# Kernel tuning notes

Measured on AMD Instinct MI355X. Metric: run time of the kernel, lower is better.

## Reference

```python
import jax, jax.numpy as jnp
import numpy as np

NEG_SLOPE = 0.2
EPS = 1e-16

def gatv2(x, edge_index, edge_attr, Wl, bl, We, att, bias):
    """PyG GATv2Conv, heads=1, share_weights=True, with edge_dim."""
    N = x.shape[0]
    h = x @ Wl + bl                      # [N, out] shared lin_l == lin_r
    src, dst = edge_index[0], edge_index[1]
    hj = h[src]                          # source (message) features [E, out]
    hi = h[dst]                          # target features [E, out]
    e = jax.nn.leaky_relu(hi + hj + edge_attr @ We, NEG_SLOPE)  # [E, out]
    score = e @ att                      # [E]
    # segment softmax over edges grouped by destination node
    smax = jax.ops.segment_max(score, dst, num_segments=N)
    ex = jnp.exp(score - smax[dst])
    denom = jax.ops.segment_sum(ex, dst, num_segments=N)
    alpha = ex / (denom[dst] + EPS)      # [E]
    out = jax.ops.segment_sum(hj * alpha[:, None], dst, num_segments=N)
    return out + bias


def setup_inputs() -> dict:
    key = jax.random.key(0)
    N, E = 50000, 800000
    D_IN, D_LAT, D_EDGE, N_ACT = 128, 128, 16, 32
    ks = jax.random.split(key, 16)
    s = 0.05
    inp = {
        "x": jax.random.normal(ks[0], (N, D_IN), jnp.float32),
        "edge_index": jax.random.randint(ks[1], (2, E), 0, N, jnp.int32),
        "edge_attr": jax.random.normal(ks[2], (E, D_EDGE), jnp.float32),
        # gnn_layer: D_IN -> D_LAT
        "Wl1": jax.random.normal(ks[3], (D_IN, D_LAT), jnp.float32) * s,
        "bl1": jnp.zeros((D_LAT,), jnp.float32),
        "We1": jax.random.normal(ks[4], (D_EDGE, D_LAT), jnp.float32) * s,
        "att1": jax.random.normal(ks[5], (D_LAT,), jnp.float32) * s,
        "bias1": jnp.zeros((D_LAT,), jnp.float32),
        # node_layer: D_LAT -> 1
        "Wl2": jax.random.normal(ks[6], (D_LAT, 1), jnp.float32) * s,
        "bl2": jnp.zeros((1,), jnp.float32),
        "We2": jax.random.normal(ks[7], (D_EDGE, 1), jnp.float32) * s,
        "att2": jax.random.normal(ks[8], (1,), jnp.float32) * s,
        "bias2": jnp.zeros((1,), jnp.float32),
        # action_layer: D_LAT -> N_ACT
        "Wl3": jax.random.normal(ks[9], (D_LAT, N_ACT), jnp.float32) * s,
        "bl3": jnp.zeros((N_ACT,), jnp.float32),
        "We3": jax.random.normal(ks[10], (D_EDGE, N_ACT), jnp.float32) * s,
        "att3": jax.random.normal(ks[11], (N_ACT,), jnp.float32) * s,
        "bias3": jnp.zeros((N_ACT,), jnp.float32),
    }
    return inp


def reference(x, edge_index, edge_attr,
              Wl1, bl1, We1, att1, bias1,
              Wl2, bl2, We2, att2, bias2,
              Wl3, bl3, We3, att3, bias3):
    latent = gatv2(x, edge_index, edge_attr, Wl1, bl1, We1, att1, bias1)          # [N, D_LAT]
    node_logits = gatv2(latent, edge_index, edge_attr, Wl2, bl2, We2, att2, bias2)[:, 0]  # [N]
    action_logits = gatv2(latent, edge_index, edge_attr, Wl3, bl3, We3, att3, bias3)      # [N, A]
    # categorical sampling with fixed key (deterministic reference)
    k1, k2 = jax.random.split(jax.random.key(42))
    node_sel = jax.random.categorical(k1, node_logits)
    node_lp = jax.nn.log_softmax(node_logits)[node_sel]
    act_logits_sel = action_logits[node_sel, :]
    action_sel = jax.random.categorical(k2, act_logits_sel)
    action_lp = jax.nn.log_softmax(act_logits_sel)[action_sel]
    return (node_sel, action_sel, node_lp + action_lp)
```

## Files before the change

### kernel.cpp

```cpp
#include <hip/hip_runtime.h>
#include <stdint.h>
#include <math.h>

#define NEG 0.2f
#define TINYF 1.1754943508222875e-38f

__host__ __device__ inline void threefry2x32(uint32_t k0, uint32_t k1,
                                             uint32_t x0, uint32_t x1,
                                             uint32_t* o0, uint32_t* o1) {
  uint32_t ks0 = k0, ks1 = k1, ks2 = k0 ^ k1 ^ 0x1BD11BDAu;
  x0 += ks0; x1 += ks1;
#define RR(r) { x0 += x1; x1 = (x1 << (r)) | (x1 >> (32 - (r))); x1 ^= x0; }
  RR(13) RR(15) RR(26) RR(6)
  x0 += ks1; x1 += ks2 + 1u;
  RR(17) RR(29) RR(16) RR(24)
  x0 += ks2; x1 += ks0 + 2u;
  RR(13) RR(15) RR(26) RR(6)
  x0 += ks0; x1 += ks1 + 3u;
  RR(17) RR(29) RR(16) RR(24)
  x0 += ks1; x1 += ks2 + 4u;
  RR(13) RR(15) RR(26) RR(6)
  x0 += ks2; x1 += ks0 + 5u;
#undef RR
  *o0 = x0; *o1 = x1;
}

__device__ inline float gumbel_part(uint32_t ka, uint32_t kb, uint32_t i) {
  uint32_t o0, o1;
  threefry2x32(ka, kb, 0u, i, &o0, &o1);
  uint32_t bits = o0 ^ o1;
  float f = __uint_as_float((bits >> 9) | 0x3f800000u) - 1.0f;
  float u = fmaxf(TINYF, f + TINYF);
  return -logf(-logf(u));
}

__global__ void count_kernel(const int* __restrict__ ei, int E, int* __restrict__ counts) {
  int e = blockIdx.x * blockDim.x + threadIdx.x;
  if (e < E) atomicAdd(&counts[ei[E + e]], 1);
}

__global__ __launch_bounds__(1024) void scan_kernel(const int* __restrict__ counts,
    int* __restrict__ row_start, int* __restrict__ cursor, int N, int E) {
  __shared__ int wsum[16];
  __shared__ int base_s;
  int tid = threadIdx.x;
  int lane = tid & 63, wv = tid >> 6;
  if (tid == 0) base_s = 0;
  __syncthreads();
  for (int chunk = 0; chunk < N; chunk += 1024) {
    int i = chunk + tid;
    int v = (i < N) ? counts[i] : 0;
    int incl = v;
#pragma unroll
    for (int off = 1; off < 64; off <<= 1) {
      int t = __shfl_up(incl, off);
      if (lane >= off) incl += t;
    }
    if (lane == 63) wsum[wv] = incl;
    __syncthreads();
    if (wv == 0) {
      int x = (lane < 16) ? wsum[lane] : 0;
#pragma unroll
      for (int off = 1; off < 16; off <<= 1) {
        int t = __shfl_up(x, off);
        if (lane >= off) x += t;
      }
      if (lane < 16) wsum[lane] = x;
    }
    __syncthreads();
    int waveoff = (wv == 0) ? 0 : wsum[wv - 1];
    int base = base_s;
    int excl = base + waveoff + incl - v;
    if (i < N) { row_start[i] = excl; cursor[i] = excl; }
    __syncthreads();
    if (tid == 1023) base_s = base + wsum[15];
    __syncthreads();
  }
  if (tid == 0) row_start[N] = base_s;
}

__global__ void scatter_kernel(const int* __restrict__ ei, const float* __restrict__ ea,
                               int E, int* __restrict__ cursor,
                               int* __restrict__ src_csr, float* __restrict__ ea_csr) {
  int e = blockIdx.x * blockDim.x + threadIdx.x;
  if (e < E) {
    int d = ei[E + e];
    int p = atomicAdd(&cursor[d], 1);
    src_csr[p] = ei[e];
    const float4* s4 = (const float4*)&ea[(size_t)e * 16];
    float4* d4 = (float4*)&ea_csr[(size_t)p * 16];
    float4 t0 = s4[0], t1 = s4[1], t2 = s4[2], t3 = s4[3];
    d4[0] = t0; d4[1] = t1; d4[2] = t2; d4[3] = t3;
  }
}

__global__ __launch_bounds__(256) void gemm128_kernel(const float* __restrict__ X,
    const float* __restrict__ W, const float* __restrict__ bias,
    float* __restrict__ out, int M) {
  __shared__ float xs[128][33];
  int row0 = blockIdx.x * 32;
  int tid = threadIdx.x;
  for (int idx = tid; idx < 32 * 128; idx += 256) {
    int r = idx >> 7;
    int k = idx & 127;
    int row = row0 + r;
    xs[k][r] = (row < M) ? X[(size_t)row * 128 + k] : 0.0f;
  }
  __syncthreads();
  int tc = tid & 31, tr = tid >> 5;
  int c0 = tc * 4, r0 = tr * 4;
  float acc[4][4] = {};
#pragma unroll 4
  for (int k = 0; k < 128; k++) {
    float4 w = *(const float4*)&W[k * 128 + c0];
    float x0 = xs[k][r0], x1 = xs[k][r0 + 1], x2 = xs[k][r0 + 2], x3 = xs[k][r0 + 3];
    acc[0][0] += x0 * w.x; acc[0][1] += x0 * w.y; acc[0][2] += x0 * w.z; acc[0][3] += x0 * w.w;
    acc[1][0] += x1 * w.x; acc[1][1] += x1 * w.y; acc[1][2] += x1 * w.z; acc[1][3] += x1 * w.w;
    acc[2][0] += x2 * w.x; acc[2][1] += x2 * w.y; acc[2][2] += x2 * w.z; acc[2][3] += x2 * w.w;
    acc[3][0] += x3 * w.x; acc[3][1] += x3 * w.y; acc[3][2] += x3 * w.z; acc[3][3] += x3 * w.w;
  }
  float4 b4 = *(const float4*)&bias[c0];
  for (int r = 0; r < 4; r++) {
    int row = row0 + r0 + r;
    if (row < M) {
      float4 o;
      o.x = acc[r][0] + b4.x; o.y = acc[r][1] + b4.y;
      o.z = acc[r][2] + b4.z; o.w = acc[r][3] + b4.w;
      *(float4*)&out[(size_t)row * 128 + c0] = o;
    }
  }
}

__global__ __launch_bounds__(256) void gemm32_kernel(const float* __restrict__ X,
    const float* __restrict__ W, const float* __restrict__ bias,
    float* __restrict__ out, int M) {
  int t = blockIdx.x * 256 + threadIdx.x;
  int node = t >> 5, c = t & 31;
  if (node >= M) return;
  const float4* xp = (const float4*)&X[(size_t)node * 128];
  float acc = 0.f;
#pragma unroll
  for (int q = 0; q < 32; q++) {
    float4 x4 = xp[q];
    acc += x4.x * W[(q * 4 + 0) * 32 + c] + x4.y * W[(q * 4 + 1) * 32 + c]
         + x4.z * W[(q * 4 + 2) * 32 + c] + x4.w * W[(q * 4 + 3) * 32 + c];
  }
  out[(size_t)node * 32 + c] = acc + bias[c];
}

__global__ __launch_bounds__(256) void gemv_kernel(const float* __restrict__ X,
    const float* __restrict__ w, const float* __restrict__ b0,
    float* __restrict__ out, int M) {
  int wv = (blockIdx.x * 256 + threadIdx.x) >> 6;
  int lane = threadIdx.x & 63;
  if (wv >= M) return;
  float2 xv = *(const float2*)&X[(size_t)wv * 128 + lane * 2];
  float2 wvv = *(const float2*)&w[lane * 2];
  float v = xv.x * wvv.x + xv.y * wvv.y;
#pragma unroll
  for (int off = 32; off; off >>= 1) v += __shfl_xor(v, off);
  if (lane == 0) out[wv] = v + b0[0];
}

__global__ __launch_bounds__(256) void fused1_kernel(const float* __restrict__ h,
    const int* __restrict__ src_csr, const int* __restrict__ row_start,
    const float* __restrict__ ea_csr,
    const float* __restrict__ We, const float* __restrict__ att,
    const float* __restrict__ bias, float* __restrict__ out, int N) {
  __shared__ float WeS[2048];
  int tid = threadIdx.x;
  for (int i = tid; i < 2048; i += 256) WeS[i] = We[i];
  __syncthreads();
  int hw = (blockIdx.x * 256 + tid) >> 5;
  int lane = tid & 31;
  if (hw >= N) return;
  int c4 = lane * 4;
  float4 attv = *(const float4*)&att[c4];
  float4 b4 = *(const float4*)&bias[c4];
  int start = row_start[hw];
  int deg = row_start[hw + 1] - start;
  if (deg == 0) {
    *(float4*)&out[(size_t)hw * 128 + c4] = b4;
    return;
  }
  float4 hi = *(const float4*)&h[(size_t)hw * 128 + c4];
  int s_l = (lane < deg) ? src_csr[start + lane] : 0;
  int dcap = deg < 32 ? deg : 32;
  const float4* eap = (const float4*)&ea_csr[(size_t)start * 16];
  float m = -INFINITY, l = 0.f;
  float4 acc = make_float4(0.f, 0.f, 0.f, 0.f);
  for (int j = 0; j < deg; j++) {
    int s = (j < dcap) ? __shfl(s_l, j, 32) : src_csr[start + j];
    float4 hj = *(const float4*)&h[(size_t)s * 128 + c4];
    float4 v;
    v.x = hi.x + hj.x; v.y = hi.y + hj.y; v.z = hi.z + hj.z; v.w = hi.w + hj.w;
#pragma unroll
    for (int q = 0; q < 4; q++) {
      float4 aq = eap[(size_t)j * 4 + q];
      float4 w0 = *(const float4*)&WeS[(4 * q + 0) * 128 + c4];
      float4 w1 = *(const float4*)&WeS[(4 * q + 1) * 128 + c4];
      float4 w2 = *(const float4*)&WeS[(4 * q + 2) * 128 + c4];
      float4 w3 = *(const float4*)&WeS[(4 * q + 3) * 128 + c4];
      v.x += aq.x * w0.x + aq.y * w1.x + aq.z * w2.x + aq.w * w3.x;
      v.y += aq.x * w0.y + aq.y * w1.y + aq.z * w2.y + aq.w * w3.y;
      v.z += aq.x * w0.z + aq.y * w1.z + aq.z * w2.z + aq.w * w3.z;
      v.w += aq.x * w0.w + aq.y * w1.w + aq.z * w2.w + aq.w * w3.w;
    }
    v.x = v.x >= 0.f ? v.x : NEG * v.x;
    v.y = v.y >= 0.f ? v.y : NEG * v.y;
    v.z = v.z >= 0.f ? v.z : NEG * v.z;
    v.w = v.w >= 0.f ? v.w : NEG * v.w;
    float sc = v.x * attv.x + v.y * attv.y + v.z * attv.z + v.w * attv.w;
#pragma unroll
    for (int off = 16; off; off >>= 1) sc += __shfl_xor(sc, off);
    float mn = fmaxf(m, sc);
    float scale = __expf(m - mn);
    float w = __expf(sc - mn);
    l = l * scale + w;
    acc.x = acc.x * scale + w * hj.x;
    acc.y = acc.y * scale + w * hj.y;
    acc.z = acc.z * scale + w * hj.z;
    acc.w = acc.w * scale + w * hj.w;
    m = mn;
  }
  float inv = 1.0f / (l + 1e-16f);
  float4 o;
  o.x = acc.x * inv + b4.x;
  o.y = acc.y * inv + b4.y;
  o.z = acc.z * inv + b4.z;
  o.w = acc.w * inv + b4.w;
  *(float4*)&out[(size_t)hw * 128 + c4] = o;
}

__global__ __launch_bounds__(256) void fused23_kernel(
    const float* __restrict__ h3, const float* __restrict__ h2,
    const int* __restrict__ src_csr, const int* __restrict__ row_start,
    const float* __restrict__ ea_csr,
    const float* __restrict__ We3, const float* __restrict__ att3,
    const float* __restrict__ bias3, const float* __restrict__ We2,
    const float* __restrict__ att2, const float* __restrict__ bias2,
    float* __restrict__ out3, float* __restrict__ logits, int N) {
  __shared__ float We3S[512];
  __shared__ float att3S[32];
  __shared__ float We2S[16];
  int tid = threadIdx.x;
  for (int i = tid; i < 512; i += 256) We3S[i] = We3[i];
  if (tid < 32) att3S[tid] = att3[tid];
  if (tid < 16) We2S[tid] = We2[tid];
  __syncthreads();
  int wv = (blockIdx.x * 256 + tid) >> 6;
  int lane = tid & 63;
  if (wv >= N) return;
  int c = lane & 31;
  int par = lane >> 5;
  float bi3 = bias3[c];
  int start = row_start[wv];
  int deg = row_start[wv + 1] - start;
  if (deg == 0) {
    if (par == 0) out3[(size_t)wv * 32 + c] = bi3;
    if (lane == 0) logits[wv] = bias2[0];
    return;
  }
  float at3 = att3S[c];
  float a2s = att2[0];
  float hi3 = h3[(size_t)wv * 32 + c];
  float hi2 = h2[wv];
  int s_l = (lane < deg) ? src_csr[start + lane] : 0;
  int dcap = deg < 64 ? deg : 64;
  const float4* eap = (const float4*)&ea_csr[(size_t)start * 16];
  float m3 = -INFINITY, l3 = 0.f, acc3 = 0.f;
  float m2 = -INFINITY, l2 = 0.f, acc2 = 0.f;
  for (int j = par; j < deg; j += 2) {
    int s = (j < dcap) ? __shfl(s_l, j) : src_csr[start + j];
    float hj3 = h3[(size_t)s * 32 + c];
    float h2s = h2[s];
    float4 c0 = eap[(size_t)j * 4 + 0];
    float4 c1 = eap[(size_t)j * 4 + 1];
    float4 c2 = eap[(size_t)j * 4 + 2];
    float4 c3 = eap[(size_t)j * 4 + 3];
    float v3 = hi3 + hj3;
    v3 += c0.x * We3S[0 * 32 + c]  + c0.y * We3S[1 * 32 + c]  + c0.z * We3S[2 * 32 + c]  + c0.w * We3S[3 * 32 + c];
    v3 += c1.x * We3S[4 * 32 + c]  + c1.y * We3S[5 * 32 + c]  + c1.z * We3S[6 * 32 + c]  + c1.w * We3S[7 * 32 + c];
    v3 += c2.x * We3S[8 * 32 + c]  + c2.y * We3S[9 * 32 + c]  + c2.z * We3S[10 * 32 + c] + c2.w * We3S[11 * 32 + c];
    v3 += c3.x * We3S[12 * 32 + c] + c3.y * We3S[13 * 32 + c] + c3.z * We3S[14 * 32 + c] + c3.w * We3S[15 * 32 + c];
    v3 = v3 >= 0.f ? v3 : NEG * v3;
    float t3 = v3 * at3;
#pragma unroll
    for (int off = 16; off; off >>= 1) t3 += __shfl_xor(t3, off);
    float v2 = hi2 + h2s;
    v2 += c0.x * We2S[0]  + c0.y * We2S[1]  + c0.z * We2S[2]  + c0.w * We2S[3];
    v2 += c1.x * We2S[4]  + c1.y * We2S[5]  + c1.z * We2S[6]  + c1.w * We2S[7];
    v2 += c2.x * We2S[8]  + c2.y * We2S[9]  + c2.z * We2S[10] + c2.w * We2S[11];
    v2 += c3.x * We2S[12] + c3.y * We2S[13] + c3.z * We2S[14] + c3.w * We2S[15];
    v2 = v2 >= 0.f ? v2 : NEG * v2;
    float t2 = v2 * a2s;
    float mn3 = fmaxf(m3, t3);
    float sc3 = __expf(m3 - mn3);
    float w3 = __expf(t3 - mn3);
    l3 = l3 * sc3 + w3;
    acc3 = acc3 * sc3 + w3 * hj3;
    m3 = mn3;
    float mn2 = fmaxf(m2, t2);
    float sc2 = __expf(m2 - mn2);
    float w2 = __expf(t2 - mn2);
    l2 = l2 * sc2 + w2;
    acc2 = acc2 * sc2 + w2 * h2s;
    m2 = mn2;
  }
  float m3o = __shfl_xor(m3, 32), l3o = __shfl_xor(l3, 32), acc3o = __shfl_xor(acc3, 32);
  float M3 = fmaxf(m3, m3o);
  float sA3 = (m3 == -INFINITY) ? 0.f : __expf(m3 - M3);
  float sB3 = (m3o == -INFINITY) ? 0.f : __expf(m3o - M3);
  float L3 = l3 * sA3 + l3o * sB3;
  float A3 = acc3 * sA3 + acc3o * sB3;
  float m2o = __shfl_xor(m2, 32), l2o = __shfl_xor(l2, 32), acc2o = __shfl_xor(acc2, 32);
  float M2 = fmaxf(m2, m2o);
  float sA2 = (m2 == -INFINITY) ? 0.f : __expf(m2 - M2);
  float sB2 = (m2o == -INFINITY) ? 0.f : __expf(m2o - M2);
  float L2 = l2 * sA2 + l2o * sB2;
  float A2 = acc2 * sA2 + acc2o * sB2;
  if (par == 0) out3[(size_t)wv * 32 + c] = A3 / (L3 + 1e-16f) + bi3;
  if (lane == 0) logits[wv] = A2 / (L2 + 1e-16f) + bias2[0];
}

#define NSB 64
__global__ __launch_bounds__(256) void node_partial_kernel(const float* __restrict__ logits,
    int N, uint32_t ka, uint32_t kb,
    float* __restrict__ pB, int* __restrict__ pI,
    float* __restrict__ pM, float* __restrict__ pL) {
  int chunk = (N + NSB - 1) / NSB;
  int s0 = blockIdx.x * chunk;
  int s1 = s0 + chunk; if (s1 > N) s1 = N;
  int tid = threadIdx.x;
  float best = -INFINITY; int bi = 0x7fffffff;
  float m = -INFINITY, l = 0.f;
  for (int i = s0 + tid; i < s1; i += 256) {
    float lg = logits[i];
    float mn = fmaxf(m, lg);
    l = l * __expf(m - mn) + __expf(lg - mn);
    m = mn;
    float v = lg + gumbel_part(ka, kb, (uint32_t)i);
    if (v > best) { best = v; bi = i; }
  }
  __shared__ float sb[256], sm[256], sl[256];
  __shared__ int si[256];
  sb[tid] = best; si[tid] = bi; sm[tid] = m; sl[tid] = l;
  __syncthreads();
  for (int s = 128; s; s >>= 1) {
    if (tid < s) {
      if (sb[tid + s] > sb[tid] || (sb[tid + s] == sb[tid] && si[tid + s] < si[tid])) {
        sb[tid] = sb[tid + s]; si[tid] = si[tid + s];
      }
      float M = fmaxf(sm[tid], sm[tid + s]);
      float t0 = (sm[tid] == -INFINITY) ? 0.f : sl[tid] * __expf(sm[tid] - M);
      float t1 = (sm[tid + s] == -INFINITY) ? 0.f : sl[tid + s] * __expf(sm[tid + s] - M);
      sm[tid] = M; sl[tid] = t0 + t1;
    }
    __syncthreads();
  }
  if (tid == 0) { pB[blockIdx.x] = sb[0]; pI[blockIdx.x] = si[0]; pM[blockIdx.x] = sm[0]; pL[blockIdx.x] = sl[0]; }
}

__global__ __launch_bounds__(64) void node_final_kernel(const float* __restrict__ logits,
    const float* __restrict__ pB, const int* __restrict__ pI,
    const float* __restrict__ pM, const float* __restrict__ pL,
    float* __restrict__ scal) {
  int lane = threadIdx.x;
  float best = pB[lane]; int bi = pI[lane];
  float m = pM[lane]; float l = pL[lane];
#pragma unroll
  for (int off = 32; off; off >>= 1) {
    float ob = __shfl_xor(best, off); int oi = __shfl_xor(bi, off);
    if (ob > best || (ob == best && oi < bi)) { best = ob; bi = oi; }
    float om = __shfl_xor(m, off); float ol = __shfl_xor(l, off);
    float M = fmaxf(m, om);
    float t0 = (m == -INFINITY) ? 0.f : l * __expf(m - M);
    float t1 = (om == -INFINITY) ? 0.f : ol * __expf(om - M);
    m = M; l = t0 + t1;
  }
  if (lane == 0) {
    ((int*)scal)[0] = bi;
    scal[3] = logits[bi] - (m + logf(l));
  }
}

__global__ __launch_bounds__(64) void action_kernel(const float* __restrict__ out3,
    const float* __restrict__ scal, uint32_t ka, uint32_t kb,
    float* __restrict__ dout, int out_size) {
  int lane = threadIdx.x;
  int sel = ((const int*)scal)[0];
  float v = -INFINITY, noisy = -INFINITY;
  if (lane < 32) {
    v = out3[(size_t)sel * 32 + lane];
    noisy = v + gumbel_part(ka, kb, (uint32_t)lane);
  }
  int idx = lane;
  float nv = noisy;
#pragma unroll
  for (int off = 32; off; off >>= 1) {
    float ov = __shfl_xor(nv, off);
    int oi = __shfl_xor(idx, off);
    if (ov > nv || (ov == nv && oi < idx)) { nv = ov; idx = oi; }
  }
  float vm = v;
#pragma unroll
  for (int off = 32; off; off >>= 1) vm = fmaxf(vm, __shfl_xor(vm, off));
  float ex = (lane < 32) ? expf(v - vm) : 0.f;
#pragma unroll
  for (int off = 32; off; off >>= 1) ex += __shfl_xor(ex, off);
  float vsel = __shfl(v, idx);
  if (lane == 0) {
    float action_lp = vsel - vm - logf(ex);
    dout[0] = (float)sel;
    dout[1] = (float)idx;
    dout[2] = scal[3] + action_lp;
  }
  for (int i = 3 + lane; i < out_size; i += 64) dout[i] = 0.f;
}

extern "C" void kernel_launch(void* const* d_in, const int* in_sizes, int n_in,
                              void* d_out, int out_size, void* d_ws, size_t ws_size,
                              hipStream_t stream) {
  const float* x     = (const float*)d_in[0];
  const int*   ei    = (const int*)d_in[1];
  const float* ea    = (const float*)d_in[2];
  const float* Wl1   = (const float*)d_in[3];
  const float* bl1   = (const float*)d_in[4];
  const float* We1   = (const float*)d_in[5];
  const float* att1  = (const float*)d_in[6];
  const float* bias1 = (const float*)d_in[7];
  const float* Wl2   = (const float*)d_in[8];
  const float* bl2   = (const float*)d_in[9];
  const float* We2   = (const float*)d_in[10];
  const float* att2  = (const float*)d_in[11];
  const float* bias2 = (const float*)d_in[12];
  const float* Wl3   = (const float*)d_in[13];
  const float* bl3   = (const float*)d_in[14];
  const float* We3   = (const float*)d_in[15];
  const float* att3  = (const float*)d_in[16];
  const float* bias3 = (const float*)d_in[17];
  int N = in_sizes[0] / 128;
  int E = in_sizes[1] / 2;
  float* out = (float*)d_out;

  char* p = (char*)d_ws;
  auto alloc = [&](size_t bytes) -> char* {
    char* r = p; p += (bytes + 255) & ~(size_t)255; return r;
  };
  float* h1      = (float*)alloc((size_t)N * 128 * 4);
  float* latent  = (float*)alloc((size_t)N * 128 * 4);
  float* h3      = (float*)alloc((size_t)N * 32 * 4);
  float* h2      = (float*)alloc((size_t)N * 4);
  float* logits  = (float*)alloc((size_t)N * 4);
  float* out3    = (float*)alloc((size_t)N * 32 * 4);
  int* counts    = (int*)alloc((size_t)N * 4);
  int* row_start = (int*)alloc((size_t)(N + 1) * 4);
  int* cursor    = (int*)alloc((size_t)N * 4);
  int* src_csr   = (int*)alloc((size_t)E * 4);
  float* ea_csr  = (float*)alloc((size_t)E * 16 * 4);
  float* pB      = (float*)alloc(NSB * 4);
  int*   pI      = (int*)alloc(NSB * 4);
  float* pM      = (float*)alloc(NSB * 4);
  float* pL      = (float*)alloc(NSB * 4);
  float* scal    = (float*)alloc(64);
  (void)ws_size; (void)n_in;

  uint32_t k1a, k1b, k2a, k2b;
  threefry2x32(0u, 42u, 0u, 0u, &k1a, &k1b);
  threefry2x32(0u, 42u, 0u, 1u, &k2a, &k2b);

  hipMemsetAsync(counts, 0, (size_t)N * 4, stream);
  count_kernel<<<(E + 255) / 256, 256, 0, stream>>>(ei, E, counts);
  scan_kernel<<<1, 1024, 0, stream>>>(counts, row_start, cursor, N, E);
  scatter_kernel<<<(E + 255) / 256, 256, 0, stream>>>(ei, ea, E, cursor, src_csr, ea_csr);

  gemm128_kernel<<<(N + 31) / 32, 256, 0, stream>>>(x, Wl1, bl1, h1, N);
  fused1_kernel<<<(N + 7) / 8, 256, 0, stream>>>(h1, src_csr, row_start,
                                                 ea_csr, We1, att1, bias1, latent, N);

  gemm32_kernel<<<((size_t)N * 32 + 255) / 256, 256, 0, stream>>>(latent, Wl3, bl3, h3, N);
  gemv_kernel<<<(N + 3) / 4, 256, 0, stream>>>(latent, Wl2, bl2, h2, N);

  fused23_kernel<<<(N + 3) / 4, 256, 0, stream>>>(h3, h2, src_csr, row_start, ea_csr,
                                                  We3, att3, bias3, We2, att2, bias2,
                                                  out3, logits, N);

  node_partial_kernel<<<NSB, 256, 0, stream>>>(logits, N, k1a, k1b, pB, pI, pM, pL);
  node_final_kernel<<<1, 64, 0, stream>>>(logits, pB, pI, pM, pL, scal);
  action_kernel<<<1, 64, 0, stream>>>(out3, scal, k2a, k2b, out, out_size);
}
```

Before: 665.8 us.

## Narrow per-node lane groups in fused edge-softmax kernels and register-cache edge weights

Layer-1 fused kernel now assigns 16 lanes per destination node with 8 channels each instead of 32 lanes with 4, so a wavefront covers four nodes and each lane issues more independent loads and FMAs. The layer-2/3 kernel splits edges across four 16-lane groups with two action channels per lane, holds We3/We2 in registers instead of LDS, and merges the online-softmax partial states through a two-step shuffle tree. The aim is more memory-level parallelism on the irregular gathers and fewer idle lanes on low-degree nodes, at the cost of higher register pressure and possibly lower occupancy.

```diff
diff --git a/kernel.cpp b/kernel.cpp
--- a/kernel.cpp
+++ b/kernel.cpp
@@ -171,65 +171,84 @@
   int tid = threadIdx.x;
   for (int i = tid; i < 2048; i += 256) WeS[i] = We[i];
   __syncthreads();
-  int hw = (blockIdx.x * 256 + tid) >> 5;
-  int lane = tid & 31;
-  if (hw >= N) return;
-  int c4 = lane * 4;
-  float4 attv = *(const float4*)&att[c4];
-  float4 b4 = *(const float4*)&bias[c4];
-  int start = row_start[hw];
-  int deg = row_start[hw + 1] - start;
+  int node = (blockIdx.x * 256 + tid) >> 4;
+  int l16 = tid & 15;
+  if (node >= N) return;
+  int c8 = l16 * 8;
+  float4 at0 = *(const float4*)&att[c8];
+  float4 at1 = *(const float4*)&att[c8 + 4];
+  float4 bb0 = *(const float4*)&bias[c8];
+  float4 bb1 = *(const float4*)&bias[c8 + 4];
+  int start = row_start[node];
+  int deg = row_start[node + 1] - start;
+  float* op = &out[(size_t)node * 128 + c8];
   if (deg == 0) {
-    *(float4*)&out[(size_t)hw * 128 + c4] = b4;
+    *(float4*)op = bb0;
+    *(float4*)(op + 4) = bb1;
     return;
   }
-  float4 hi = *(const float4*)&h[(size_t)hw * 128 + c4];
-  int s_l = (lane < deg) ? src_csr[start + lane] : 0;
-  int dcap = deg < 32 ? deg : 32;
+  const float4* hp0 = (const float4*)&h[(size_t)node * 128 + c8];
+  float4 hi0 = hp0[0], hi1 = hp0[1];
+  int s_l = (l16 < deg) ? src_csr[start + l16] : 0;
+  int dcap = deg < 16 ? deg : 16;
   const float4* eap = (const float4*)&ea_csr[(size_t)start * 16];
   float m = -INFINITY, l = 0.f;
-  float4 acc = make_float4(0.f, 0.f, 0.f, 0.f);
+  float4 acc0 = make_float4(0.f, 0.f, 0.f, 0.f);
+  float4 acc1 = make_float4(0.f, 0.f, 0.f, 0.f);
   for (int j = 0; j < deg; j++) {
-    int s = (j < dcap) ? __shfl(s_l, j, 32) : src_csr[start + j];
-    float4 hj = *(const float4*)&h[(size_t)s * 128 + c4];
-    float4 v;
-    v.x = hi.x + hj.x; v.y = hi.y + hj.y; v.z = hi.z + hj.z; v.w = hi.w + hj.w;
+    int s = (j < dcap) ? __shfl(s_l, j, 16) : src_csr[start + j];
+    const float4* hjp = (const float4*)&h[(size_t)s * 128 + c8];
+    float4 hj0 = hjp[0], hj1 = hjp[1];
+    float4 v0, v1;
+    v0.x = hi0.x + hj0.x; v0.y = hi0.y + hj0.y; v0.z = hi0.z + hj0.z; v0.w = hi0.w + hj0.w;
+    v1.x = hi1.x + hj1.x; v1.y = hi1.y + hj1.y; v1.z = hi1.z + hj1.z; v1.w = hi1.w + hj1.w;
 #pragma unroll
     for (int q = 0; q < 4; q++) {
       float4 aq = eap[(size_t)j * 4 + q];
-      float4 w0 = *(const float4*)&WeS[(4 * q + 0) * 128 + c4];
-      float4 w1 = *(const float4*)&WeS[(4 * q + 1) * 128 + c4];
-      float4 w2 = *(const float4*)&WeS[(4 * q + 2) * 128 + c4];
-      float4 w3 = *(const float4*)&WeS[(4 * q + 3) * 128 + c4];
-      v.x += aq.x * w0.x + aq.y * w1.x + aq.z * w2.x + aq.w * w3.x;
-      v.y += aq.x * w0.y + aq.y * w1.y + aq.z * w2.y + aq.w * w3.y;
-      v.z += aq.x * w0.z + aq.y * w1.z + aq.z * w2.z + aq.w * w3.z;
-      v.w += aq.x * w0.w + aq.y * w1.w + aq.z * w2.w + aq.w * w3.w;
+#pragma unroll
+      for (int r = 0; r < 4; r++) {
+        int k = 4 * q + r;
+        float a = (r == 0) ? aq.x : (r == 1) ? aq.y : (r == 2) ? aq.z : aq.w;
+        float4 wa = *(const float4*)&WeS[k * 128 + c8];
+        float4 wb = *(const float4*)&WeS[k * 128 + c8 + 4];
+        v0.x += a * wa.x; v0.y += a * wa.y; v0.z += a * wa.z; v0.w += a * wa.w;
+        v1.x += a * wb.x; v1.y += a * wb.y; v1.z += a * wb.z; v1.w += a * wb.w;
+      }
     }
-    v.x = v.x >= 0.f ? v.x : NEG * v.x;
-    v.y = v.y >= 0.f ? v.y : NEG * v.y;
-    v.z = v.z >= 0.f ? v.z : NEG * v.z;
-    v.w = v.w >= 0.f ? v.w : NEG * v.w;
-    float sc = v.x * attv.x + v.y * attv.y + v.z * attv.z + v.w * attv.w;
-#pragma unroll
-    for (int off = 16; off; off >>= 1) sc += __shfl_xor(sc, off);
+    v0.x = v0.x >= 0.f ? v0.x : NEG * v0.x;
+    v0.y = v0.y >= 0.f ? v0.y : NEG * v0.y;
+    v0.z = v0.z >= 0.f ? v0.z : NEG * v0.z;
+    v0.w = v0.w >= 0.f ? v0.w : NEG * v0.w;
+    v1.x = v1.x >= 0.f ? v1.x : NEG * v1.x;
+    v1.y = v1.y >= 0.f ? v1.y : NEG * v1.y;
+    v1.z = v1.z >= 0.f ? v1.z : NEG * v1.z;
+    v1.w = v1.w >= 0.f ? v1.w : NEG * v1.w;
+    float sc = v0.x * at0.x + v0.y * at0.y + v0.z * at0.z + v0.w * at0.w
+             + v1.x * at1.x + v1.y * at1.y + v1.z * at1.z + v1.w * at1.w;
+#pragma unroll
+    for (int off = 8; off; off >>= 1) sc += __shfl_xor(sc, off);
     float mn = fmaxf(m, sc);
     float scale = __expf(m - mn);
     float w = __expf(sc - mn);
     l = l * scale + w;
-    acc.x = acc.x * scale + w * hj.x;
-    acc.y = acc.y * scale + w * hj.y;
-    acc.z = acc.z * scale + w * hj.z;
-    acc.w = acc.w * scale + w * hj.w;
+    acc0.x = acc0.x * scale + w * hj0.x;
+    acc0.y = acc0.y * scale + w * hj0.y;
+    acc0.z = acc0.z * scale + w * hj0.z;
+    acc0.w = acc0.w * scale + w * hj0.w;
+    acc1.x = acc1.x * scale + w * hj1.x;
+    acc1.y = acc1.y * scale + w * hj1.y;
+    acc1.z = acc1.z * scale + w * hj1.z;
+    acc1.w = acc1.w * scale + w * hj1.w;
     m = mn;
   }
   float inv = 1.0f / (l + 1e-16f);
-  float4 o;
-  o.x = acc.x * inv + b4.x;
-  o.y = acc.y * inv + b4.y;
-  o.z = acc.z * inv + b4.z;
-  o.w = acc.w * inv + b4.w;
-  *(float4*)&out[(size_t)hw * 128 + c4] = o;
+  float4 o0, o1;
+  o0.x = acc0.x * inv + bb0.x; o0.y = acc0.y * inv + bb0.y;
+  o0.z = acc0.z * inv + bb0.z; o0.w = acc0.w * inv + bb0.w;
+  o1.x = acc1.x * inv + bb1.x; o1.y = acc1.y * inv + bb1.y;
+  o1.z = acc1.z * inv + bb1.z; o1.w = acc1.w * inv + bb1.w;
+  *(float4*)op = o0;
+  *(float4*)(op + 4) = o1;
 }
 
 __global__ __launch_bounds__(256) void fused23_kernel(
@@ -240,87 +259,106 @@
     const float* __restrict__ bias3, const float* __restrict__ We2,
     const float* __restrict__ att2, const float* __restrict__ bias2,
     float* __restrict__ out3, float* __restrict__ logits, int N) {
-  __shared__ float We3S[512];
-  __shared__ float att3S[32];
-  __shared__ float We2S[16];
   int tid = threadIdx.x;
-  for (int i = tid; i < 512; i += 256) We3S[i] = We3[i];
-  if (tid < 32) att3S[tid] = att3[tid];
-  if (tid < 16) We2S[tid] = We2[tid];
-  __syncthreads();
   int wv = (blockIdx.x * 256 + tid) >> 6;
   int lane = tid & 63;
   if (wv >= N) return;
-  int c = lane & 31;
-  int par = lane >> 5;
-  float bi3 = bias3[c];
+  int q4 = lane >> 4;
+  int l16 = lane & 15;
+  int c2 = l16 * 2;
+  float2 we3[16];
+#pragma unroll
+  for (int k = 0; k < 16; k++) we3[k] = *(const float2*)&We3[k * 32 + c2];
+  float we2[16];
+#pragma unroll
+  for (int k = 0; k < 16; k++) we2[k] = We2[k];
+  float2 at3 = *(const float2*)&att3[c2];
+  float a2s = att2[0];
+  float2 bi3 = *(const float2*)&bias3[c2];
   int start = row_start[wv];
   int deg = row_start[wv + 1] - start;
   if (deg == 0) {
-    if (par == 0) out3[(size_t)wv * 32 + c] = bi3;
+    if (lane < 16) *(float2*)&out3[(size_t)wv * 32 + c2] = bi3;
     if (lane == 0) logits[wv] = bias2[0];
     return;
   }
-  float at3 = att3S[c];
-  float a2s = att2[0];
-  float hi3 = h3[(size_t)wv * 32 + c];
+  float2 hi3 = *(const float2*)&h3[(size_t)wv * 32 + c2];
   float hi2 = h2[wv];
   int s_l = (lane < deg) ? src_csr[start + lane] : 0;
   int dcap = deg < 64 ? deg : 64;
   const float4* eap = (const float4*)&ea_csr[(size_t)start * 16];
-  float m3 = -INFINITY, l3 = 0.f, acc3 = 0.f;
-  float m2 = -INFINITY, l2 = 0.f, acc2 = 0.f;
-  for (int j = par; j < deg; j += 2) {
+  float m3 = -INFINITY, l3 = 0.f; float2 a3 = make_float2(0.f, 0.f);
+  float m2 = -INFINITY, l2 = 0.f; float a2 = 0.f;
+  for (int j = q4; j < deg; j += 4) {
     int s = (j < dcap) ? __shfl(s_l, j) : src_csr[start + j];
-    float hj3 = h3[(size_t)s * 32 + c];
+    float2 hj3 = *(const float2*)&h3[(size_t)s * 32 + c2];
     float h2s = h2[s];
     float4 c0 = eap[(size_t)j * 4 + 0];
     float4 c1 = eap[(size_t)j * 4 + 1];
-    float4 c2 = eap[(size_t)j * 4 + 2];
+    float4 cc2 = eap[(size_t)j * 4 + 2];
     float4 c3 = eap[(size_t)j * 4 + 3];
-    float v3 = hi3 + hj3;
-    v3 += c0.x * We3S[0 * 32 + c]  + c0.y * We3S[1 * 32 + c]  + c0.z * We3S[2 * 32 + c]  + c0.w * We3S[3 * 32 + c];
-    v3 += c1.x * We3S[4 * 32 + c]  + c1.y * We3S[5 * 32 + c]  + c1.z * We3S[6 * 32 + c]  + c1.w * We3S[7 * 32 + c];
-    v3 += c2.x * We3S[8 * 32 + c]  + c2.y * We3S[9 * 32 + c]  + c2.z * We3S[10 * 32 + c] + c2.w * We3S[11 * 32 + c];
-    v3 += c3.x * We3S[12 * 32 + c] + c3.y * We3S[13 * 32 + c] + c3.z * We3S[14 * 32 + c] + c3.w * We3S[15 * 32 + c];
-    v3 = v3 >= 0.f ? v3 : NEG * v3;
-    float t3 = v3 * at3;
-#pragma unroll
-    for (int off = 16; off; off >>= 1) t3 += __shfl_xor(t3, off);
+    float vx = hi3.x + hj3.x, vy = hi3.y + hj3.y;
+    vx += c0.x * we3[0].x + c0.y * we3[1].x + c0.z * we3[2].x + c0.w * we3[3].x;
+    vy += c0.x * we3[0].y + c0.y * we3[1].y + c0.z * we3[2].y + c0.w * we3[3].y;
+    vx += c1.x * we3[4].x + c1.y * we3[5].x + c1.z * we3[6].x + c1.w * we3[7].x;
+    vy += c1.x * we3[4].y + c1.y * we3[5].y + c1.z * we3[6].y + c1.w * we3[7].y;
+    vx += cc2.x * we3[8].x + cc2.y * we3[9].x + cc2.z * we3[10].x + cc2.w * we3[11].x;
+    vy += cc2.x * we3[8].y + cc2.y * we3[9].y + cc2.z * we3[10].y + cc2.w * we3[11].y;
+    vx += c3.x * we3[12].x + c3.y * we3[13].x + c3.z * we3[14].x + c3.w * we3[15].x;
+    vy += c3.x * we3[12].y + c3.y * we3[13].y + c3.z * we3[14].y + c3.w * we3[15].y;
+    vx = vx >= 0.f ? vx : NEG * vx;
+    vy = vy >= 0.f ? vy : NEG * vy;
+    float t3 = vx * at3.x + vy * at3.y;
+#pragma unroll
+    for (int off = 8; off; off >>= 1) t3 += __shfl_xor(t3, off);
     float v2 = hi2 + h2s;
-    v2 += c0.x * We2S[0]  + c0.y * We2S[1]  + c0.z * We2S[2]  + c0.w * We2S[3];
-    v2 += c1.x * We2S[4]  + c1.y * We2S[5]  + c1.z * We2S[6]  + c1.w * We2S[7];
-    v2 += c2.x * We2S[8]  + c2.y * We2S[9]  + c2.z * We2S[10] + c2.w * We2S[11];
-    v2 += c3.x * We2S[12] + c3.y * We2S[13] + c3.z * We2S[14] + c3.w * We2S[15];
+    v2 += c0.x * we2[0]  + c0.y * we2[1]  + c0.z * we2[2]  + c0.w * we2[3];
+    v2 += c1.x * we2[4]  + c1.y * we2[5]  + c1.z * we2[6]  + c1.w * we2[7];
+    v2 += cc2.x * we2[8] + cc2.y * we2[9] + cc2.z * we2[10] + cc2.w * we2[11];
+    v2 += c3.x * we2[12] + c3.y * we2[13] + c3.z * we2[14] + c3.w * we2[15];
     v2 = v2 >= 0.f ? v2 : NEG * v2;
     float t2 = v2 * a2s;
     float mn3 = fmaxf(m3, t3);
     float sc3 = __expf(m3 - mn3);
     float w3 = __expf(t3 - mn3);
     l3 = l3 * sc3 + w3;
-    acc3 = acc3 * sc3 + w3 * hj3;
+    a3.x = a3.x * sc3 + w3 * hj3.x;
+    a3.y = a3.y * sc3 + w3 * hj3.y;
     m3 = mn3;
     float mn2 = fmaxf(m2, t2);
     float sc2 = __expf(m2 - mn2);
     float w2 = __expf(t2 - mn2);
     l2 = l2 * sc2 + w2;
-    acc2 = acc2 * sc2 + w2 * h2s;
+    a2 = a2 * sc2 + w2 * h2s;
     m2 = mn2;
   }
-  float m3o = __shfl_xor(m3, 32), l3o = __shfl_xor(l3, 32), acc3o = __shfl_xor(acc3, 32);
-  float M3 = fmaxf(m3, m3o);
-  float sA3 = (m3 == -INFINITY) ? 0.f : __expf(m3 - M3);
-  float sB3 = (m3o == -INFINITY) ? 0.f : __expf(m3o - M3);
-  float L3 = l3 * sA3 + l3o * sB3;
-  float A3 = acc3 * sA3 + acc3o * sB3;
-  float m2o = __shfl_xor(m2, 32), l2o = __shfl_xor(l2, 32), acc2o = __shfl_xor(acc2, 32);
-  float M2 = fmaxf(m2, m2o);
-  float sA2 = (m2 == -INFINITY) ? 0.f : __expf(m2 - M2);
-  float sB2 = (m2o == -INFINITY) ? 0.f : __expf(m2o - M2);
-  float L2 = l2 * sA2 + l2o * sB2;
-  float A2 = acc2 * sA2 + acc2o * sB2;
-  if (par == 0) out3[(size_t)wv * 32 + c] = A3 / (L3 + 1e-16f) + bi3;
-  if (lane == 0) logits[wv] = A2 / (L2 + 1e-16f) + bias2[0];
+#pragma unroll
+  for (int off = 16; off <= 32; off <<= 1) {
+    float m3o = __shfl_xor(m3, off), l3o = __shfl_xor(l3, off);
+    float ax = __shfl_xor(a3.x, off), ay = __shfl_xor(a3.y, off);
+    float M3 = fmaxf(m3, m3o);
+    float sA = (m3 == -INFINITY) ? 0.f : __expf(m3 - M3);
+    float sB = (m3o == -INFINITY) ? 0.f : __expf(m3o - M3);
+    l3 = l3 * sA + l3o * sB;
+    a3.x = a3.x * sA + ax * sB;
+    a3.y = a3.y * sA + ay * sB;
+    m3 = M3;
+    float m2o = __shfl_xor(m2, off), l2o = __shfl_xor(l2, off);
+    float az = __shfl_xor(a2, off);
+    float M2 = fmaxf(m2, m2o);
+    float tA = (m2 == -INFINITY) ? 0.f : __expf(m2 - M2);
+    float tB = (m2o == -INFINITY) ? 0.f : __expf(m2o - M2);
+    l2 = l2 * tA + l2o * tB;
+    a2 = a2 * tA + az * tB;
+    m2 = M2;
+  }
+  if (lane < 16) {
+    float2 o;
+    o.x = a3.x / (l3 + 1e-16f) + bi3.x;
+    o.y = a3.y / (l3 + 1e-16f) + bi3.y;
+    *(float2*)&out3[(size_t)wv * 32 + c2] = o;
+  }
+  if (lane == 0) logits[wv] = a2 / (l2 + 1e-16f) + bias2[0];
 }
 
 #define NSB 64
@@ -475,8 +513,8 @@
   scatter_kernel<<<(E + 255) / 256, 256, 0, stream>>>(ei, ea, E, cursor, src_csr, ea_csr);
 
   gemm128_kernel<<<(N + 31) / 32, 256, 0, stream>>>(x, Wl1, bl1, h1, N);
-  fused1_kernel<<<(N + 7) / 8, 256, 0, stream>>>(h1, src_csr, row_start,
-                                                 ea_csr, We1, att1, bias1, latent, N);
+  fused1_kernel<<<(N + 15) / 16, 256, 0, stream>>>(h1, src_csr, row_start,
+                                                   ea_csr, We1, att1, bias1, latent, N);
 
   gemm32_kernel<<<((size_t)N * 32 + 255) / 256, 256, 0, stream>>>(latent, Wl3, bl3, h3, N);
   gemv_kernel<<<(N + 3) / 4, 256, 0, stream>>>(latent, Wl2, bl2, h2, N);
```

New measurement: 752.7 us. 13.1% more time.
